# Kernel tuning notes

Hardware: AMD Instinct MI355X
Metric: run time of the kernel (lower is better)

The kernel has to match this reference:

```python
import jax, jax.numpy as jnp
import numpy as np

D_MODEL = 768
N_HEADS = 12
D_FF = 3072
EPS = 1e-6


def _xavier(key, shape):
    fan_out, fan_in = shape
    a = jnp.sqrt(6.0 / (fan_in + fan_out))
    return jax.random.uniform(key, shape, jnp.float32, -a, a)


def setup_inputs() -> dict:
    key = jax.random.key(0)
    ks = jax.random.split(key, 10)
    B, S = 2, 2048
    x = jax.random.normal(ks[0], (B, S, D_MODEL), jnp.float32)
    mask = jax.random.randint(ks[1], (B, 1, 1, S), 0, 2) == 1
    wq = _xavier(ks[2], (D_MODEL, D_MODEL)); bq = jnp.zeros((D_MODEL,))
    wk = _xavier(ks[3], (D_MODEL, D_MODEL)); bk = jnp.zeros((D_MODEL,))
    wv = _xavier(ks[4], (D_MODEL, D_MODEL)); bv = jnp.zeros((D_MODEL,))
    wo = _xavier(ks[5], (D_MODEL, D_MODEL)); bo = jnp.zeros((D_MODEL,))
    w1 = _xavier(ks[6], (D_FF, D_MODEL)); b1 = jnp.zeros((D_FF,))
    w2 = _xavier(ks[7], (D_MODEL, D_FF)); b2 = jnp.zeros((D_MODEL,))
    g1 = jnp.ones((D_MODEL,)); be1 = jnp.zeros((D_MODEL,))
    g2 = jnp.ones((D_MODEL,)); be2 = jnp.zeros((D_MODEL,))
    return dict(x=x, mask=mask, wq=wq, bq=bq, wk=wk, bk=bk, wv=wv, bv=bv,
                wo=wo, bo=bo, w1=w1, b1=b1, w2=w2, b2=b2,
                g1=g1, be1=be1, g2=g2, be2=be2)


def _layer_norm(x, gamma, beta):
    # torch: mean + unbiased std (ddof=1), divide by (std + eps)
    mean = jnp.mean(x, axis=-1, keepdims=True)
    std = jnp.std(x, axis=-1, keepdims=True, ddof=1)
    return gamma * (x - mean) / (std + EPS) + beta


def _encoder(x, mask, wq, bq, wk, bk, wv, bv, wo, bo, w1, b1, w2, b2, g1, be1, g2, be2):
    B, S, D = x.shape
    H, Dk = N_HEADS, D // N_HEADS
    q = (x @ wq.T + bq).reshape(B, S, H, Dk).transpose(0, 2, 1, 3)
    k = (x @ wk.T + bk).reshape(B, S, H, Dk).transpose(0, 2, 1, 3)
    v = (x @ wv.T + bv).reshape(B, S, H, Dk).transpose(0, 2, 1, 3)
    scores = jnp.einsum('bhqd,bhkd->bhqk', q, k) / jnp.sqrt(jnp.float32(Dk))
    scores = jnp.where(mask, jnp.float32(-1e9), scores)
    probs = jax.nn.softmax(scores, axis=-1)
    attn = jnp.einsum('bhqk,bhkd->bhqd', probs, v)
    attn = attn.transpose(0, 2, 1, 3).reshape(B, S, D)
    attn = attn @ wo.T + bo
    x = _layer_norm(x + attn, g1, be1)
    ff = jax.nn.relu(x @ w1.T + b1) @ w2.T + b2
    return _layer_norm(x + ff, g2, be2)


def reference(x, mask, wq, bq, wk, bk, wv, bv, wo, bo, w1, b1, w2, b2, g1, be1, g2, be2):
    return _encoder(x, mask, wq, bq, wk, bk, wv, bv, wo, bo, w1, b1, w2, b2, g1, be1, g2, be2)
```

## Files before the change

kernel.cpp:

```cpp
#include <hip/hip_runtime.h>
#include <hip/hip_bf16.h>

typedef __hip_bfloat16 bf16;
typedef unsigned short ushort;
typedef __attribute__((ext_vector_type(8))) short short8;
typedef __attribute__((ext_vector_type(4))) float f32x4;

__device__ __forceinline__ float b2f(bf16 h) { return __bfloat162float(h); }
__device__ __forceinline__ bf16 f2b(float f) { return __float2bfloat16(f); }
__device__ __forceinline__ ushort f2bu(float f) {
    bf16 t = __float2bfloat16(f);
    ushort u;
    __builtin_memcpy(&u, &t, 2);
    return u;
}
__device__ __forceinline__ float bits2f(unsigned int u16) {
    unsigned int v = u16 << 16;
    float f;
    __builtin_memcpy(&f, &v, 4);
    return f;
}

__device__ __forceinline__ void gload16(const void* g, void* l) {
    __builtin_amdgcn_global_load_lds(
        (const __attribute__((address_space(1))) void*)g,
        (__attribute__((address_space(3))) void*)l, 16, 0, 0);
}

__global__ void detect_dtype_kernel(const unsigned short* __restrict__ x,
                                    int* __restrict__ flag) {
    __shared__ int cnt;
    if (threadIdx.x == 0) cnt = 0;
    __syncthreads();
    int local = 0;
    for (int i = threadIdx.x; i < 2048; i += 256) {
        float v = bits2f((unsigned int)x[i]);
        if (!(fabsf(v) < 1e4f)) local++;
    }
    atomicAdd(&cnt, local);
    __syncthreads();
    if (threadIdx.x == 0) flag[0] = (cnt >= 8) ? 1 : 0;
}

__device__ __forceinline__ void load8f_rt(const void* p, int isf, float* f) {
    if (isf) {
        const float* q = (const float*)p;
        float4 a = *(const float4*)q;
        float4 b = *(const float4*)(q + 4);
        f[0] = a.x; f[1] = a.y; f[2] = a.z; f[3] = a.w;
        f[4] = b.x; f[5] = b.y; f[6] = b.z; f[7] = b.w;
    } else {
        uint4 u = *(const uint4*)p;
        f[0] = bits2f(u.x & 0xffffu); f[1] = bits2f(u.x >> 16);
        f[2] = bits2f(u.y & 0xffffu); f[3] = bits2f(u.y >> 16);
        f[4] = bits2f(u.z & 0xffffu); f[5] = bits2f(u.z >> 16);
        f[6] = bits2f(u.w & 0xffffu); f[7] = bits2f(u.w >> 16);
    }
}
__device__ __forceinline__ float loadf_rt(const void* p, int isf, size_t i) {
    return isf ? ((const float*)p)[i] : bits2f(((const ushort*)p)[i]);
}

__global__ __launch_bounds__(256) void conv_all_k(
    const int* __restrict__ dflag,
    const void* __restrict__ x,
    const void* __restrict__ wq, const void* __restrict__ wk,
    const void* __restrict__ wv, const void* __restrict__ wo,
    const void* __restrict__ w1, const void* __restrict__ w2,
    const void* __restrict__ bq, const void* __restrict__ bk,
    const void* __restrict__ bv, const void* __restrict__ bo,
    const void* __restrict__ b1, const void* __restrict__ b2,
    const void* __restrict__ g1, const void* __restrict__ be1,
    const void* __restrict__ g2, const void* __restrict__ be2,
    ushort* __restrict__ xb, ushort* __restrict__ wall,
    float* __restrict__ vall)
{
    const int isf = dflag[0];
    const int esz = isf ? 4 : 2;
    const int gt = blockIdx.x * 256 + threadIdx.x;
    const int stride = gridDim.x * 256;

    for (int v = gt; v < 393216; v += stride) {
        float f[8];
        load8f_rt((const char*)x + (size_t)v * 8 * esz, isf, f);
        unsigned int wd[4];
        #pragma unroll
        for (int i = 0; i < 4; ++i)
            wd[i] = (unsigned int)f2bu(f[2 * i]) | ((unsigned int)f2bu(f[2 * i + 1]) << 16);
        *(uint4*)(xb + (size_t)v * 8) = make_uint4(wd[0], wd[1], wd[2], wd[3]);
    }
    for (int v = gt; v < 884736; v += stride) {
        const void* src; int loc;
        if (v < 73728)        { src = wq; loc = v; }
        else if (v < 147456)  { src = wk; loc = v - 73728; }
        else if (v < 221184)  { src = wv; loc = v - 147456; }
        else if (v < 294912)  { src = wo; loc = v - 221184; }
        else if (v < 589824)  { src = w1; loc = v - 294912; }
        else                  { src = w2; loc = v - 589824; }
        float f[8];
        load8f_rt((const char*)src + (size_t)loc * 8 * esz, isf, f);
        unsigned int wd[4];
        #pragma unroll
        for (int i = 0; i < 4; ++i)
            wd[i] = (unsigned int)f2bu(f[2 * i]) | ((unsigned int)f2bu(f[2 * i + 1]) << 16);
        *(uint4*)(wall + (size_t)v * 8) = make_uint4(wd[0], wd[1], wd[2], wd[3]);
    }
    for (int i = gt; i < 9984; i += stride) {
        const void* s; int l;
        if (i < 768)       { s = bq;  l = i; }
        else if (i < 1536) { s = bk;  l = i - 768; }
        else if (i < 2304) { s = bv;  l = i - 1536; }
        else if (i < 3072) { s = bo;  l = i - 2304; }
        else if (i < 6144) { s = b1;  l = i - 3072; }
        else if (i < 6912) { s = b2;  l = i - 6144; }
        else if (i < 7680) { s = g1;  l = i - 6912; }
        else if (i < 8448) { s = be1; l = i - 7680; }
        else if (i < 9216) { s = g2;  l = i - 8448; }
        else               { s = be2; l = i - 9216; }
        vall[i] = loadf_rt(s, isf, l);
    }
}

template <int BM>
__device__ __forceinline__ void gemm_bf16_body(
    const ushort* __restrict__ A, const ushort* __restrict__ Bw,
    const float* __restrict__ bias, ushort* __restrict__ Cb,
    float* __restrict__ Cf, int N, int K, int bm, int bn, int relu)
{
    __shared__ __align__(16) ushort As[BM][64];
    __shared__ __align__(16) ushort Bs[128][64];
    const int tid = threadIdx.x;
    const int w = tid >> 6, lane = tid & 63;
    const int quad = lane >> 4, l15 = lane & 15;
    constexpr int FM = BM / 32;
    const int wr = (w >> 1) * (BM / 2), wc = (w & 1) * 64;

    constexpr int CA = (BM * 128) / 4096;
    constexpr int CB = 4;
    size_t aoff[CA]; int albase[CA];
    #pragma unroll
    for (int c = 0; c < CA; ++c) {
        int byte = c * 4096 + tid * 16;
        int row = byte >> 7, colb = byte & 127;
        int csrc = colb ^ ((row & 7) << 4);
        aoff[c] = (size_t)(bm + row) * K + (csrc >> 1);
        albase[c] = c * 4096 + w * 1024;
    }
    size_t boff[CB]; int blbase[CB];
    #pragma unroll
    for (int c = 0; c < CB; ++c) {
        int byte = c * 4096 + tid * 16;
        int row = byte >> 7, colb = byte & 127;
        int csrc = colb ^ ((row & 7) << 4);
        boff[c] = (size_t)(bn + row) * K + (csrc >> 1);
        blbase[c] = c * 4096 + w * 1024;
    }

    f32x4 acc[FM][4];
    #pragma unroll
    for (int i = 0; i < FM; ++i)
        #pragma unroll
        for (int j = 0; j < 4; ++j) acc[i][j] = (f32x4){0.f, 0.f, 0.f, 0.f};

    char* AsB = (char*)&As[0][0];
    char* BsB = (char*)&Bs[0][0];

    for (int k0 = 0; k0 < K; k0 += 64) {
        __syncthreads();
        #pragma unroll
        for (int c = 0; c < CA; ++c)
            gload16(A + aoff[c] + k0, AsB + albase[c]);
        #pragma unroll
        for (int c = 0; c < CB; ++c)
            gload16(Bw + boff[c] + k0, BsB + blbase[c]);
        __syncthreads();

        short8 af[FM][2], bfr[4][2];
        #pragma unroll
        for (int i = 0; i < FM; ++i) {
            int r = wr + i * 16 + l15;
            int sw = (r & 7) << 3;
            af[i][0] = *(const short8*)&As[r][(quad * 8) ^ sw];
            af[i][1] = *(const short8*)&As[r][(32 + quad * 8) ^ sw];
        }
        #pragma unroll
        for (int j = 0; j < 4; ++j) {
            int r = wc + j * 16 + l15;
            int sw = (r & 7) << 3;
            bfr[j][0] = *(const short8*)&Bs[r][(quad * 8) ^ sw];
            bfr[j][1] = *(const short8*)&Bs[r][(32 + quad * 8) ^ sw];
        }
        #pragma unroll
        for (int h = 0; h < 2; ++h)
            #pragma unroll
            for (int i = 0; i < FM; ++i)
                #pragma unroll
                for (int j = 0; j < 4; ++j)
                    acc[i][j] = __builtin_amdgcn_mfma_f32_16x16x32_bf16(
                        af[i][h], bfr[j][h], acc[i][j], 0, 0, 0);
    }

    #pragma unroll
    for (int j = 0; j < 4; ++j) {
        int col = bn + wc + j * 16 + l15;
        float bv = bias[col];
        #pragma unroll
        for (int i = 0; i < FM; ++i) {
            int row0 = bm + wr + i * 16 + quad * 4;
            #pragma unroll
            for (int r = 0; r < 4; ++r) {
                float vv = acc[i][j][r] + bv;
                if (relu) vv = fmaxf(vv, 0.f);
                size_t idx = (size_t)(row0 + r) * N + col;
                if (Cb) Cb[idx] = f2bu(vv);
                if (Cf) Cf[idx] = vv;
            }
        }
    }
}

__device__ __forceinline__ int xcd_swz(int bid, int nwg) {
    int cpx = nwg >> 3;
    return (bid & 7) * cpx + (bid >> 3);
}

template <int BM>
__global__ __launch_bounds__(256) void gemm_b(
    const ushort* __restrict__ A, const ushort* __restrict__ Bw,
    const float* __restrict__ bias, ushort* __restrict__ Cb,
    float* __restrict__ Cf, int N, int K, int relu)
{
    int nwg = gridDim.x * gridDim.y;
    int bid = xcd_swz(blockIdx.y * gridDim.x + blockIdx.x, nwg);
    int bx = bid % gridDim.x, by = bid / gridDim.x;
    gemm_bf16_body<BM>(A, Bw, bias, Cb, Cf, N, K, by * BM, bx * 128, relu);
}

__global__ __launch_bounds__(256) void gemm_qkv_b(
    const ushort* __restrict__ x, const ushort* __restrict__ wall,
    const float* __restrict__ vall,
    ushort* __restrict__ qb, ushort* __restrict__ kb, ushort* __restrict__ vb)
{
    int bid = xcd_swz(blockIdx.y * 18 + blockIdx.x, 576);
    int bx = bid % 18, by = bid / 18;
    const int mat = bx / 6;
    const int bn = (bx % 6) * 128;
    const ushort* W = wall + (size_t)mat * 589824;
    const float* Bi = vall + mat * 768;
    ushort* O = (mat == 0) ? qb : (mat == 1) ? kb : vb;
    gemm_bf16_body<128>(x, W, Bi, O, nullptr, 768, 768, by * 128, bn, 0);
}

__global__ __launch_bounds__(512) void attn_mfma_b(
    const ushort* __restrict__ q, const ushort* __restrict__ k,
    const ushort* __restrict__ v, const int* __restrict__ mask,
    float* __restrict__ opart, float* __restrict__ mlbuf)
{
    const int S = 2048, D = 768;
    const size_t NXD = 3145728;
    const float SC2 = 0.125f * 1.44269504088896f;
    __shared__ __align__(16) ushort Ks[64][72];
    __shared__ __align__(16) ushort Vt[64][72];
    __shared__ __align__(16) ushort Ps[8][16][72];
    __shared__ float mkAll[1024];

    const int tid = threadIdx.x;
    const int w = tid >> 6, lane = tid & 63;
    const int quad = lane >> 4, l15 = lane & 15;

    const int bx = blockIdx.x;
    const int part = bx / 384;
    const int rest = bx - part * 384;
    const int q0 = (rest & 15) * 128;
    const int h = (rest >> 4) % 12;
    const int b = rest / 192;
    const int kbase = part * 1024;

    #pragma unroll
    for (int i = 0; i < 2; ++i) {
        int idx = tid + i * 512;
        mkAll[idx] = mask[b * S + kbase + idx] ? -30000.f : 0.f;
    }

    const size_t qrow = (size_t)(b * S + q0 + w * 16 + l15) * D + h * 64;
    const short8 aQ0 = *(const short8*)&q[qrow + quad * 8];
    const short8 aQ1 = *(const short8*)&q[qrow + 32 + quad * 8];

    short8 ones;
    #pragma unroll
    for (int j = 0; j < 8; ++j) ones[j] = (short)0x3F80;

    f32x4 o[4], lacc;
    #pragma unroll
    for (int i = 0; i < 4; ++i) o[i] = (f32x4){0.f, 0.f, 0.f, 0.f};
    lacc = (f32x4){0.f, 0.f, 0.f, 0.f};
    float m_run = -3.0e38f;

    const int sr = tid >> 3;
    const int sc0 = (tid & 7) * 8;

    const ushort* kp = k + (size_t)(b * S + kbase + sr) * D + h * 64 + sc0;
    const ushort* vp = v + (size_t)(b * S + kbase + lane) * D + h * 64 + w * 8;
    uint4 ka = *(const uint4*)kp;
    uint4 va = *(const uint4*)vp;

    for (int kt = 0; kt < 16; ++kt) {
        __syncthreads();
        *(uint4*)&Ks[sr][sc0] = ka;
        {
            alignas(16) ushort tmp[8];
            *(uint4*)tmp = va;
            #pragma unroll
            for (int i = 0; i < 8; ++i) Vt[w * 8 + i][lane] = tmp[i];
        }
        __syncthreads();

        if (kt + 1 < 16) {
            kp += 64 * D;
            vp += 64 * D;
            ka = *(const uint4*)kp;
            va = *(const uint4*)vp;
        }

        const float* mk = &mkAll[kt * 64];
        float scv[4][4];
        float vm = -3.0e38f;
        #pragma unroll
        for (int s = 0; s < 4; ++s) {
            short8 bk0 = *(const short8*)&Ks[s * 16 + l15][quad * 8];
            short8 bk1 = *(const short8*)&Ks[s * 16 + l15][32 + quad * 8];
            f32x4 c = (f32x4){0.f, 0.f, 0.f, 0.f};
            c = __builtin_amdgcn_mfma_f32_16x16x32_bf16(aQ0, bk0, c, 0, 0, 0);
            c = __builtin_amdgcn_mfma_f32_16x16x32_bf16(aQ1, bk1, c, 0, 0, 0);
            float mb = mk[s * 16 + l15];
            #pragma unroll
            for (int r = 0; r < 4; ++r) {
                float val = __builtin_fmaf(c[r], SC2, mb);
                scv[s][r] = val;
                vm = fmaxf(vm, val);
            }
        }
        vm = fmaxf(vm, __shfl_xor(vm, 1, 16));
        vm = fmaxf(vm, __shfl_xor(vm, 2, 16));
        vm = fmaxf(vm, __shfl_xor(vm, 4, 16));
        vm = fmaxf(vm, __shfl_xor(vm, 8, 16));

        if (__any(vm > m_run + 11.0f)) {
            float mn = fmaxf(m_run, vm);
            float alpha = exp2f(m_run - mn);
            #pragma unroll
            for (int s = 0; s < 4; ++s) o[s] *= alpha;
            lacc *= alpha;
            m_run = mn;
        }

        #pragma unroll
        for (int r = 0; r < 4; ++r)
            #pragma unroll
            for (int s = 0; s < 4; ++s)
                Ps[w][quad * 4 + r][(s * 16 + l15) ^ (quad << 4)] =
                    f2bu(exp2f(scv[s][r] - m_run));
        asm volatile("s_waitcnt lgkmcnt(0)" ::: "memory");

        {
            const int pswz = (l15 >> 2) << 4;
            short8 aP0 = *(const short8*)&Ps[w][l15][(quad * 8) ^ pswz];
            short8 aP1 = *(const short8*)&Ps[w][l15][(32 + quad * 8) ^ pswz];
            lacc = __builtin_amdgcn_mfma_f32_16x16x32_bf16(aP0, ones, lacc, 0, 0, 0);
            lacc = __builtin_amdgcn_mfma_f32_16x16x32_bf16(aP1, ones, lacc, 0, 0, 0);
            #pragma unroll
            for (int s = 0; s < 4; ++s) {
                short8 bv0 = *(const short8*)&Vt[s * 16 + l15][quad * 8];
                short8 bv1 = *(const short8*)&Vt[s * 16 + l15][32 + quad * 8];
                o[s] = __builtin_amdgcn_mfma_f32_16x16x32_bf16(aP0, bv0, o[s], 0, 0, 0);
                o[s] = __builtin_amdgcn_mfma_f32_16x16x32_bf16(aP1, bv1, o[s], 0, 0, 0);
            }
        }
    }

    const size_t obase = (size_t)part * NXD +
                         (size_t)(b * S + q0 + w * 16) * D + h * 64;
    #pragma unroll
    for (int r = 0; r < 4; ++r)
        #pragma unroll
        for (int s = 0; s < 4; ++s)
            opart[obase + (size_t)(quad * 4 + r) * D + s * 16 + l15] = o[s][r];
    if (l15 == 0) {
        #pragma unroll
        for (int r = 0; r < 4; ++r) {
            int row = b * S + q0 + w * 16 + quad * 4 + r;
            size_t mi = (((size_t)part * 4096 + row) * 12 + h) * 2;
            mlbuf[mi] = m_run;
            mlbuf[mi + 1] = lacc[r];
        }
    }
}

__global__ __launch_bounds__(256) void attn_combine(
    const float* __restrict__ opart, const float* __restrict__ mlbuf,
    ushort* __restrict__ ctx)
{
    const size_t NXD = 3145728;
    const int row = blockIdx.x;
    const int tid = threadIdx.x;
    #pragma unroll
    for (int i = 0; i < 3; ++i) {
        int d = tid + i * 256;
        int h = d >> 6;
        size_t m0i = ((size_t)row * 12 + h) * 2;
        size_t m1i = (((size_t)4096 + row) * 12 + h) * 2;
        float m0 = mlbuf[m0i], l0 = mlbuf[m0i + 1];
        float m1 = mlbuf[m1i], l1 = mlbuf[m1i + 1];
        float m = fmaxf(m0, m1);
        float e0 = exp2f(m0 - m), e1 = exp2f(m1 - m);
        float inv = 1.f / (l0 * e0 + l1 * e1);
        size_t idx = (size_t)row * 768 + d;
        float val = (opart[idx] * e0 + opart[NXD + idx] * e1) * inv;
        ctx[idx] = f2bu(val);
    }
}

__global__ __launch_bounds__(256) void ln1_kernel(
    const int* __restrict__ dflag,
    const void* __restrict__ xa, const float* __restrict__ r,
    const float* __restrict__ gamma, const float* __restrict__ beta,
    ushort* __restrict__ outb, float* __restrict__ outf)
{
    const int isf = dflag[0];
    const int row = blockIdx.x;
    const int tid = threadIdx.x;
    __shared__ float red[4];
    const size_t base = (size_t)row * 768;

    float x[3];
    #pragma unroll
    for (int i = 0; i < 3; ++i) {
        int d = tid + i * 256;
        x[i] = loadf_rt(xa, isf, base + d) + r[base + d];
    }

    float s = x[0] + x[1] + x[2];
    #pragma unroll
    for (int off = 32; off > 0; off >>= 1) s += __shfl_down(s, off, 64);
    if ((tid & 63) == 0) red[tid >> 6] = s;
    __syncthreads();
    float mean = (red[0] + red[1] + red[2] + red[3]) * (1.f / 768.f);
    __syncthreads();

    float vsum = 0.f;
    #pragma unroll
    for (int i = 0; i < 3; ++i) {
        float dd = x[i] - mean;
        vsum += dd * dd;
    }
    #pragma unroll
    for (int off = 32; off > 0; off >>= 1) vsum += __shfl_down(vsum, off, 64);
    if ((tid & 63) == 0) red[tid >> 6] = vsum;
    __syncthreads();
    float var = (red[0] + red[1] + red[2] + red[3]) * (1.f / 767.f);
    float inv = 1.f / (sqrtf(var) + 1e-6f);

    #pragma unroll
    for (int i = 0; i < 3; ++i) {
        int d = tid + i * 256;
        float y = gamma[d] * (x[i] - mean) * inv + beta[d];
        outb[base + d] = f2bu(y);
        outf[base + d] = y;
    }
}

__global__ __launch_bounds__(256) void ln2_kernel(
    const int* __restrict__ dflag,
    const float* __restrict__ a, const float* __restrict__ r,
    const float* __restrict__ gamma, const float* __restrict__ beta,
    void* __restrict__ out)
{
    const int isf = dflag[0];
    const int row = blockIdx.x;
    const int tid = threadIdx.x;
    __shared__ float red[4];
    const size_t base = (size_t)row * 768;

    float x[3];
    #pragma unroll
    for (int i = 0; i < 3; ++i) {
        int d = tid + i * 256;
        x[i] = a[base + d] + r[base + d];
    }

    float s = x[0] + x[1] + x[2];
    #pragma unroll
    for (int off = 32; off > 0; off >>= 1) s += __shfl_down(s, off, 64);
    if ((tid & 63) == 0) red[tid >> 6] = s;
    __syncthreads();
    float mean = (red[0] + red[1] + red[2] + red[3]) * (1.f / 768.f);
    __syncthreads();

    float vsum = 0.f;
    #pragma unroll
    for (int i = 0; i < 3; ++i) {
        float dd = x[i] - mean;
        vsum += dd * dd;
    }
    #pragma unroll
    for (int off = 32; off > 0; off >>= 1) vsum += __shfl_down(vsum, off, 64);
    if ((tid & 63) == 0) red[tid >> 6] = vsum;
    __syncthreads();
    float var = (red[0] + red[1] + red[2] + red[3]) * (1.f / 767.f);
    float inv = 1.f / (sqrtf(var) + 1e-6f);

    #pragma unroll
    for (int i = 0; i < 3; ++i) {
        int d = tid + i * 256;
        float y = gamma[d] * (x[i] - mean) * inv + beta[d];
        if (isf) ((float*)out)[base + d] = y;
        else     ((ushort*)out)[base + d] = f2bu(y);
    }
}

extern "C" void kernel_launch(void* const* d_in, const int* in_sizes, int n_in,
                              void* d_out, int out_size, void* d_ws, size_t ws_size,
                              hipStream_t stream) {
    const size_t nxd = 3145728;
    char* base = (char*)d_ws;
    int* dflag = (int*)base;

    char* p = base + 256;
    ushort* xb   = (ushort*)p; p += nxd * 2;
    ushort* wall = (ushort*)p; p += 7077888ull * 2;
    float*  vall = (float*)p;  p += 40960;
    ushort* qb   = (ushort*)p;
    ushort* kb   = qb + nxd;
    ushort* vb   = kb + nxd;
    ushort* ctx  = vb + nxd;
    ushort* ff1b = qb;
    p += 4 * nxd * 2;
    float* oproj = (float*)p;
    float* ff2f  = oproj;
    p += nxd * 4;
    ushort* ln1b = (ushort*)p; p += nxd * 2;
    float*  ln1f = (float*)p;  p += nxd * 4;

    float* opart = oproj;
    float* mlbuf = oproj + 2 * nxd;

    const int* mask = (const int*)d_in[1];
    dim3 blk(256);

    detect_dtype_kernel<<<dim3(1), blk, 0, stream>>>(
        (const unsigned short*)d_in[0], dflag);

    conv_all_k<<<dim3(1024), blk, 0, stream>>>(dflag,
        d_in[0], d_in[2], d_in[4], d_in[6], d_in[8], d_in[10], d_in[12],
        d_in[3], d_in[5], d_in[7], d_in[9], d_in[11], d_in[13],
        d_in[14], d_in[15], d_in[16], d_in[17], xb, wall, vall);

    gemm_qkv_b<<<dim3(18, 32), blk, 0, stream>>>(xb, wall, vall, qb, kb, vb);

    attn_mfma_b<<<dim3(768), dim3(512), 0, stream>>>(qb, kb, vb, mask, opart, mlbuf);
    attn_combine<<<dim3(4096), blk, 0, stream>>>(opart, mlbuf, ctx);

    gemm_b<64><<<dim3(6, 64), blk, 0, stream>>>(
        ctx, wall + 1769472, vall + 2304, nullptr, oproj, 768, 768, 0);

    ln1_kernel<<<dim3(4096), blk, 0, stream>>>(dflag,
        d_in[0], oproj, vall + 6912, vall + 7680, ln1b, ln1f);

    gemm_b<128><<<dim3(24, 32), blk, 0, stream>>>(
        ln1b, wall + 2359296, vall + 3072, ff1b, nullptr, 3072, 768, 1);

    gemm_b<64><<<dim3(6, 64), blk, 0, stream>>>(
        ff1b, wall + 4718592, vall + 6144, nullptr, ff2f, 768, 3072, 0);

    ln2_kernel<<<dim3(4096), blk, 0, stream>>>(dflag,
        ln1f, ff2f, vall + 8448, vall + 9216, d_out);
}
```

Measured before the change: 332.7 us.

## Double-buffer GEMM LDS tiles and raise MFMA wave priority in attention

The bf16 GEMM body now keeps two LDS buffers for the A and B tiles. It issues the global-to-LDS loads for tile k+1 before computing on tile k, so one barrier per iteration replaces two and load latency overlaps with MFMA work. The attention kernel wraps its QK^T and PV MFMA sections in s_setprio(1)/s_setprio(0) so those waves get scheduling priority. The extra buffer doubles GEMM shared memory, which can lower occupancy. The overlap only helps if the compiler does not insert a conservative vmcnt wait before the LDS reads.

Result: faster. 324.7 us (-2.4%).

```diff
diff --git a/kernel.cpp b/kernel.cpp
--- a/kernel.cpp
+++ b/kernel.cpp
@@ -127,8 +127,8 @@
     const float* __restrict__ bias, ushort* __restrict__ Cb,
     float* __restrict__ Cf, int N, int K, int bm, int bn, int relu)
 {
-    __shared__ __align__(16) ushort As[BM][64];
-    __shared__ __align__(16) ushort Bs[128][64];
+    __shared__ __align__(16) ushort As[2][BM][64];
+    __shared__ __align__(16) ushort Bs[2][128][64];
     const int tid = threadIdx.x;
     const int w = tid >> 6, lane = tid & 63;
     const int quad = lane >> 4, l15 = lane & 15;
@@ -162,33 +162,44 @@
         #pragma unroll
         for (int j = 0; j < 4; ++j) acc[i][j] = (f32x4){0.f, 0.f, 0.f, 0.f};
 
-    char* AsB = (char*)&As[0][0];
-    char* BsB = (char*)&Bs[0][0];
-
-    for (int k0 = 0; k0 < K; k0 += 64) {
+    constexpr int ASZ = BM * 128;
+    constexpr int BSZ = 128 * 128;
+
+#define STAGE(buf, k0)                                                        \
+    {                                                                         \
+        char* ab = (char*)As + (buf) * ASZ;                                   \
+        char* bb = (char*)Bs + (buf) * BSZ;                                   \
+        _Pragma("unroll")                                                     \
+        for (int c = 0; c < CA; ++c)                                          \
+            gload16(A + aoff[c] + (k0), ab + albase[c]);                      \
+        _Pragma("unroll")                                                     \
+        for (int c = 0; c < CB; ++c)                                          \
+            gload16(Bw + boff[c] + (k0), bb + blbase[c]);                     \
+    }
+
+    const int NT = K >> 6;
+    STAGE(0, 0);
+    int cur = 0;
+    for (int t = 0; t < NT; ++t) {
         __syncthreads();
-        #pragma unroll
-        for (int c = 0; c < CA; ++c)
-            gload16(A + aoff[c] + k0, AsB + albase[c]);
-        #pragma unroll
-        for (int c = 0; c < CB; ++c)
-            gload16(Bw + boff[c] + k0, BsB + blbase[c]);
-        __syncthreads();
-
+        if (t + 1 < NT) STAGE(cur ^ 1, (t + 1) * 64);
+
+        const ushort (*Asb)[64] = As[cur];
+        const ushort (*Bsb)[64] = Bs[cur];
         short8 af[FM][2], bfr[4][2];
         #pragma unroll
         for (int i = 0; i < FM; ++i) {
             int r = wr + i * 16 + l15;
             int sw = (r & 7) << 3;
-            af[i][0] = *(const short8*)&As[r][(quad * 8) ^ sw];
-            af[i][1] = *(const short8*)&As[r][(32 + quad * 8) ^ sw];
+            af[i][0] = *(const short8*)&Asb[r][(quad * 8) ^ sw];
+            af[i][1] = *(const short8*)&Asb[r][(32 + quad * 8) ^ sw];
         }
         #pragma unroll
         for (int j = 0; j < 4; ++j) {
             int r = wc + j * 16 + l15;
             int sw = (r & 7) << 3;
-            bfr[j][0] = *(const short8*)&Bs[r][(quad * 8) ^ sw];
-            bfr[j][1] = *(const short8*)&Bs[r][(32 + quad * 8) ^ sw];
+            bfr[j][0] = *(const short8*)&Bsb[r][(quad * 8) ^ sw];
+            bfr[j][1] = *(const short8*)&Bsb[r][(32 + quad * 8) ^ sw];
         }
         #pragma unroll
         for (int h = 0; h < 2; ++h)
@@ -198,7 +209,9 @@
                 for (int j = 0; j < 4; ++j)
                     acc[i][j] = __builtin_amdgcn_mfma_f32_16x16x32_bf16(
                         af[i][h], bfr[j][h], acc[i][j], 0, 0, 0);
-    }
+        cur ^= 1;
+    }
+#undef STAGE
 
     #pragma unroll
     for (int j = 0; j < 4; ++j) {
@@ -325,6 +338,7 @@
         const float* mk = &mkAll[kt * 64];
         float scv[4][4];
         float vm = -3.0e38f;
+        __builtin_amdgcn_s_setprio(1);
         #pragma unroll
         for (int s = 0; s < 4; ++s) {
             short8 bk0 = *(const short8*)&Ks[s * 16 + l15][quad * 8];
@@ -340,6 +354,7 @@
                 vm = fmaxf(vm, val);
             }
         }
+        __builtin_amdgcn_s_setprio(0);
         vm = fmaxf(vm, __shfl_xor(vm, 1, 16));
         vm = fmaxf(vm, __shfl_xor(vm, 2, 16));
         vm = fmaxf(vm, __shfl_xor(vm, 4, 16));
@@ -366,6 +381,7 @@
             const int pswz = (l15 >> 2) << 4;
             short8 aP0 = *(const short8*)&Ps[w][l15][(quad * 8) ^ pswz];
             short8 aP1 = *(const short8*)&Ps[w][l15][(32 + quad * 8) ^ pswz];
+            __builtin_amdgcn_s_setprio(1);
             lacc = __builtin_amdgcn_mfma_f32_16x16x32_bf16(aP0, ones, lacc, 0, 0, 0);
             lacc = __builtin_amdgcn_mfma_f32_16x16x32_bf16(aP1, ones, lacc, 0, 0, 0);
             #pragma unroll
@@ -375,6 +391,7 @@
                 o[s] = __builtin_amdgcn_mfma_f32_16x16x32_bf16(aP0, bv0, o[s], 0, 0, 0);
                 o[s] = __builtin_amdgcn_mfma_f32_16x16x32_bf16(aP1, bv1, o[s], 0, 0, 0);
             }
+            __builtin_amdgcn_s_setprio(0);
         }
     }
 
```
